# Kernel tuning notes

Measured on AMD Instinct MI355X. Metric: run time of the kernel, lower is better.

Reference implementation:

```python
import jax, jax.numpy as jnp
import numpy as np

B, T, TC = 128, 300, 20          # batch, words per sentence, chars per word
DW, DC = 16, 32                  # word / char embedding dims
UC, UM = 32, 64                  # char-LSTM units, main-LSTM units
POS, PAR = 20, 8                 # extra feature dims
VW, VC = 1834, 132               # vocab sizes
DIN = DW + UC + POS + PAR        # 76, input dim of main BiLSTM


def setup_inputs() -> dict:
    key = jax.random.key(0)
    ks = jax.random.split(key, 16)
    s = 0.05
    f32 = jnp.float32
    return dict(
        word_in=jax.random.randint(ks[0], (B, T), 0, VW, dtype=jnp.int32),
        char_in=jax.random.randint(ks[1], (B, T, TC), 0, VC, dtype=jnp.int32),
        input_pos=jax.random.normal(ks[2], (B, T, POS), f32),
        input_par=jax.random.normal(ks[3], (B, T, PAR), f32),
        emb_wor=jax.random.normal(ks[4], (VW, DW), f32) * s,
        emb_char=jax.random.normal(ks[5], (VC, DC), f32) * s,
        char_Wx=jax.random.normal(ks[6], (DC, 4 * UC), f32) * s,
        char_Wh=jax.random.normal(ks[7], (UC, 4 * UC), f32) * s,
        char_b=jnp.zeros((4 * UC,), f32),
        fwd_Wx=jax.random.normal(ks[8], (DIN, 4 * UM), f32) * s,
        fwd_Wh=jax.random.normal(ks[9], (UM, 4 * UM), f32) * s,
        fwd_b=jnp.zeros((4 * UM,), f32),
        bwd_Wx=jax.random.normal(ks[10], (DIN, 4 * UM), f32) * s,
        bwd_Wh=jax.random.normal(ks[11], (UM, 4 * UM), f32) * s,
        bwd_b=jnp.zeros((4 * UM,), f32),
        dense_W=jax.random.normal(ks[12], (2 * UM, 4), f32) * s,
        dense_b=jnp.zeros((4,), f32),
    )


def _lstm(x, mask, Wx, Wh, b):
    """Masked Keras-style LSTM (gate order i,f,g,o). x:(N,S,D) mask:(N,S) bool.
    Masked steps carry state (Keras mask_zero semantics). Returns (N,S,U)."""
    U = Wh.shape[0]
    xz = jnp.einsum('nsd,df->nsf', x, Wx) + b  # hoist input projection out of scan

    def step(carry, inp):
        h, c = carry
        z_x, m = inp
        z = z_x + h @ Wh
        i, f, g, o = jnp.split(z, 4, axis=-1)
        c_new = jax.nn.sigmoid(f) * c + jax.nn.sigmoid(i) * jnp.tanh(g)
        h_new = jax.nn.sigmoid(o) * jnp.tanh(c_new)
        m = m[:, None]
        h = jnp.where(m, h_new, h)
        c = jnp.where(m, c_new, c)
        return (h, c), h

    N = x.shape[0]
    h0 = jnp.zeros((N, U), x.dtype)
    (_, _), hs = jax.lax.scan(step, (h0, h0),
                              (jnp.swapaxes(xz, 0, 1), jnp.swapaxes(mask, 0, 1)))
    return jnp.swapaxes(hs, 0, 1)


def reference(word_in, char_in, input_pos, input_par,
              emb_wor, emb_char, char_Wx, char_Wh, char_b,
              fwd_Wx, fwd_Wh, fwd_b, bwd_Wx, bwd_Wh, bwd_b,
              dense_W, dense_b):
    # word embeddings: (B,T,DW)
    ew = emb_wor[word_in]
    # char embeddings, TimeDistributed over words: (B*T, TC, DC)
    ec = emb_char[char_in].reshape(B * T, TC, DC)
    cmask = (char_in != 0).reshape(B * T, TC)
    # char LSTM, return_sequences=False -> final (last-valid) state
    ch = _lstm(ec, cmask, char_Wx, char_Wh, char_b)[:, -1, :].reshape(B, T, UC)
    # concat word emb, char encoding, extra features -> (B,T,DIN)
    x = jnp.concatenate([ew, ch, input_pos, input_par], axis=-1)
    wmask = word_in != 0
    hf = _lstm(x, wmask, fwd_Wx, fwd_Wh, fwd_b)
    hb = _lstm(x[:, ::-1], wmask[:, ::-1], bwd_Wx, bwd_Wh, bwd_b)[:, ::-1]
    h = jnp.concatenate([hf, hb], axis=-1)  # (B,T,2*UM)
    return jax.nn.softmax(h @ dense_W + dense_b, axis=-1)  # (B,T,4)
```

## Files before the change

kernel.cpp:

```cpp
#include <hip/hip_runtime.h>
#include <hip/hip_bf16.h>

#define B_ 128
#define T_ 300
#define TC_ 20
#define DW_ 16
#define DC_ 32
#define UC_ 32
#define UM_ 64
#define POS_ 20
#define PAR_ 8
#define VW_ 1834
#define VC_ 132
#define DIN_ 76
#define XS_ 80
#define NROW (B_*T_)

typedef _Float16 half_t;
typedef half_t h2 __attribute__((ext_vector_type(2)));

__device__ __forceinline__ float fast_sig(float x){
  return __builtin_amdgcn_rcpf(1.f + __expf(-x));
}
__device__ __forceinline__ float fast_tanh(float x){
  return __builtin_amdgcn_rcpf(1.f + __expf(-2.f*x))*2.f - 1.f;
}
__device__ __forceinline__ float dot2u(unsigned int a, unsigned int b, float acc){
  union{unsigned int u; h2 h;} x, y; x.u = a; y.u = b;
#if __has_builtin(__builtin_amdgcn_fdot2)
  return __builtin_amdgcn_fdot2(x.h, y.h, acc, false);
#else
  return acc + (float)x.h.x*(float)y.h.x + (float)x.h.y*(float)y.h.y;
#endif
}
__device__ __forceinline__ float us2f(unsigned short s){
  union{unsigned short s; half_t h;} x; x.s = s; return (float)x.h;
}
__device__ __forceinline__ unsigned int packh2(float a, float b){
  union{h2 h; unsigned int u;} cv; cv.h = h2{(half_t)a,(half_t)b}; return cv.u;
}

__global__ void k_prep(const float* __restrict__ emb_char, const float* __restrict__ char_Wx,
                       const float* __restrict__ char_b,  const float* __restrict__ char_Wh,
                       const float* __restrict__ Whf, const float* __restrict__ Whb,
                       const float* __restrict__ Wxf, const float* __restrict__ Wxb,
                       float* __restrict__ xzc, half_t* __restrict__ chT,
                       half_t* __restrict__ whT_h, half_t* __restrict__ wxT_h){
  int id = blockIdx.x*256 + threadIdx.x;
  if (id < 16896){
    int v = id >> 7, j = id & 127;
    float acc = char_b[j];
    #pragma unroll
    for (int k=0;k<DC_;k++) acc += emb_char[v*DC_+k]*char_Wx[k*(4*UC_)+j];
    xzc[id] = acc;
  } else if (id < 20992){
    int t = id - 16896;
    int j = t >> 5, k = t & 31;
    chT[t] = (half_t)char_Wh[k*(4*UC_)+j];
  } else if (id < 53760){
    int t = id - 20992;
    int dirr = t >> 14, j = (t >> 6) & 255, k = t & 63;
    const float* W = dirr ? Whb : Whf;
    whT_h[t] = (half_t)W[k*(4*UM_)+j];
  } else {
    int t = id - 53760;
    int dirr = t / 24576;
    int r = t % 24576;
    int jj = r / 96, k = r % 96;
    const float* W = dirr ? Wxb : Wxf;
    wxT_h[t] = (k < DIN_) ? (half_t)W[k*(4*UM_)+jj] : (half_t)0.f;
  }
}

__global__ __launch_bounds__(512,2) void k_char(const int* __restrict__ char_in,
        const float* __restrict__ xzc, const half_t* __restrict__ chT,
        const int* __restrict__ word_in, const float* __restrict__ emb_wor,
        const float* __restrict__ pos, const float* __restrict__ par,
        float* __restrict__ x){
  __shared__ unsigned int hbuf2[8][16];
  __shared__ float2 zex[8][64];
  __shared__ int sidx[8*TC_];
  const int tid = threadIdx.x;
  const int w8 = tid >> 6;
  const int lane = tid & 63;
  const int u = lane & 31;
  const int half = lane >> 5;
  const int seq = blockIdx.x*8 + w8;

  if (tid < 384){
    int r8 = tid / 48, c48 = tid % 48;
    int row = blockIdx.x*8 + r8;
    int col = (c48 < 16) ? c48 : (c48 + 32);
    float v;
    if (col < DW_)              v = emb_wor[word_in[row]*DW_ + col];
    else if (col < DW_+UC_+POS_) v = pos[row*POS_ + (col-(DW_+UC_))];
    else                         v = par[row*PAR_ + (col-(DW_+UC_+POS_))];
    x[row*XS_ + col] = v;
  }

  if (tid < 8*TC_) sidx[tid] = char_in[blockIdx.x*(8*TC_) + tid];
  if (half==0 && u<16) hbuf2[w8][u] = 0;

  unsigned int wa[16], wb[16];
  {
    const uint4* pa = reinterpret_cast<const uint4*>(chT + (half*64+u)*32);
    const uint4* pb = reinterpret_cast<const uint4*>(chT + (half*64+32+u)*32);
    #pragma unroll
    for (int q=0;q<4;q++){
      uint4 va = pa[q], vb = pb[q];
      wa[q*4+0]=va.x; wa[q*4+1]=va.y; wa[q*4+2]=va.z; wa[q*4+3]=va.w;
      wb[q*4+0]=vb.x; wb[q*4+1]=vb.y; wb[q*4+2]=vb.z; wb[q*4+3]=vb.w;
    }
  }
  __syncthreads();

  float h = 0.f, c = 0.f;
  int idx = sidx[w8*TC_ + 0];
  float za0 = xzc[idx*(4*UC_) + half*64 + u];
  float zb0 = xzc[idx*(4*UC_) + half*64 + 32 + u];

  for (int t=0; t<TC_; t++){
    int idxn = (t+1 < TC_) ? sidx[w8*TC_ + t+1] : 0;
    float zan = xzc[idxn*(4*UC_) + half*64 + u];
    float zbn = xzc[idxn*(4*UC_) + half*64 + 32 + u];

    float za = za0, zb = zb0;
    const uint4* hb = reinterpret_cast<const uint4*>(&hbuf2[w8][0]);
    uint4 q0=hb[0], q1=hb[1], q2=hb[2], q3=hb[3];
    unsigned int hu[16] = {q0.x,q0.y,q0.z,q0.w, q1.x,q1.y,q1.z,q1.w,
                           q2.x,q2.y,q2.z,q2.w, q3.x,q3.y,q3.z,q3.w};
    #pragma unroll
    for (int k=0;k<16;k++){
      za = dot2u(wa[k], hu[k], za);
      zb = dot2u(wb[k], hu[k], zb);
    }
    zex[w8][lane] = make_float2(za, zb);
    if (half == 0){
      float2 p = zex[w8][32+u];
      float zi = za, zf = zb, zg = p.x, zo = p.y;
      float cn = fast_sig(zf)*c + fast_sig(zi)*fast_tanh(zg);
      float hn = fast_sig(zo)*fast_tanh(cn);
      bool m = (idx != 0);
      c = m ? cn : c;
      h = m ? hn : h;
      reinterpret_cast<half_t*>(&hbuf2[w8][0])[u] = (half_t)h;
    }
    idx = idxn; za0 = zan; zb0 = zbn;
  }
  if (half == 0) x[seq*XS_ + DW_ + u] = h;
}

__global__ __launch_bounds__(512,2) void k_xz(const float* __restrict__ x,
      const half_t* __restrict__ wxT_h,
      const float* __restrict__ b_f, const float* __restrict__ b_b,
      half_t* __restrict__ xz){
  __shared__ unsigned int xs[16][40];
  const int j = threadIdx.x;
  const int jj = j & 255;
  const bool bwd = (j >= 256);
  const float bj = bwd ? b_b[jj] : b_f[jj];
  const int u = jj & 63, g = jj >> 6;
  const int ocol = (bwd ? 256 : 0) + u*4 + g;

  unsigned int wq[40];
  {
    const uint4* p = reinterpret_cast<const uint4*>(wxT_h + (size_t)((bwd?256:0)+jj)*96);
    #pragma unroll
    for (int q=0;q<10;q++){
      uint4 v = p[q];
      wq[q*4+0]=v.x; wq[q*4+1]=v.y; wq[q*4+2]=v.z; wq[q*4+3]=v.w;
    }
  }

  const int rowbase = blockIdx.x*16;
  for (int i=j; i<16*40; i+=512){
    int r = i/40, q = i%40;
    unsigned int pk = 0;
    if (q < 38){
      float v0 = x[(size_t)(rowbase+r)*XS_ + 2*q];
      float v1 = x[(size_t)(rowbase+r)*XS_ + 2*q+1];
      pk = packh2(v0, v1);
    }
    xs[r][q] = pk;
  }
  __syncthreads();

  for (int r=0; r<16; r++){
    const uint4* xr = reinterpret_cast<const uint4*>(&xs[r][0]);
    float acc = bj;
    #pragma unroll
    for (int q=0;q<10;q++){
      uint4 v = xr[q];
      acc = dot2u(wq[q*4+0], v.x, acc);
      acc = dot2u(wq[q*4+1], v.y, acc);
      acc = dot2u(wq[q*4+2], v.z, acc);
      acc = dot2u(wq[q*4+3], v.w, acc);
    }
    xz[(size_t)(rowbase+r)*512 + ocol] = (half_t)acc;
  }
}

__global__ __launch_bounds__(64,1) void k_rnn(const half_t* __restrict__ xz,
      const int* __restrict__ word_in, const half_t* __restrict__ whT_h,
      half_t* __restrict__ hcat){
  __shared__ half_t hbuf[64];
  __shared__ int wm[T_];
  const int l = threadIdx.x;
  const int dir = blockIdx.x & 1;
  const int b = blockIdx.x >> 1;

  unsigned int wt[4][32];
  #pragma unroll
  for (int g=0; g<4; g++){
    const uint4* p = reinterpret_cast<const uint4*>(whT_h + ((size_t)dir*256 + g*64 + l)*64);
    #pragma unroll
    for (int q=0;q<8;q++){
      uint4 v = p[q];
      wt[g][q*4+0]=v.x; wt[g][q*4+1]=v.y; wt[g][q*4+2]=v.z; wt[g][q*4+3]=v.w;
    }
  }
  for (int t=l; t<T_; t+=64) wm[t] = word_in[b*T_ + (dir ? (T_-1-t) : t)];
  hbuf[l] = (half_t)0.f;
  __syncthreads();

  float h = 0.f, c_ = 0.f;
  int row0 = b*T_ + (dir ? T_-1 : 0);
  const half_t* xp = xz + (size_t)row0*512 + dir*256 + l*4;
  const ptrdiff_t dstep = dir ? -512 : 512;
  half_t* hout = hcat + (size_t)row0*(2*UM_) + dir*UM_ + l;
  const ptrdiff_t hstep = dir ? -(2*UM_) : (2*UM_);

  ushort4 z0 = *reinterpret_cast<const ushort4*>(xp);
  ushort4 z1 = *reinterpret_cast<const ushort4*>(xp + dstep);
  half_t hh[10];

  for (int outer=0; outer<30; ++outer){
    #pragma unroll
    for (int s=0; s<10; ++s){
      const int t = outer*10 + s;
      ushort4 z2 = {0,0,0,0};
      if (t+2 < T_) z2 = *reinterpret_cast<const ushort4*>(xp + 2*dstep);

      const uint4* hb = reinterpret_cast<const uint4*>(hbuf);
      float ai0=0.f, ai1=0.f, af0=0.f, af1=0.f;
      float ag0=0.f, ag1=0.f, ao0=0.f, ao1=0.f;
      #pragma unroll
      for (int q=0;q<8;q++){
        uint4 hv = hb[q];
        ai0 = dot2u(wt[0][q*4+0], hv.x, ai0); ai1 = dot2u(wt[0][q*4+1], hv.y, ai1);
        ai0 = dot2u(wt[0][q*4+2], hv.z, ai0); ai1 = dot2u(wt[0][q*4+3], hv.w, ai1);
        af0 = dot2u(wt[1][q*4+0], hv.x, af0); af1 = dot2u(wt[1][q*4+1], hv.y, af1);
        af0 = dot2u(wt[1][q*4+2], hv.z, af0); af1 = dot2u(wt[1][q*4+3], hv.w, af1);
        ag0 = dot2u(wt[2][q*4+0], hv.x, ag0); ag1 = dot2u(wt[2][q*4+1], hv.y, ag1);
        ag0 = dot2u(wt[2][q*4+2], hv.z, ag0); ag1 = dot2u(wt[2][q*4+3], hv.w, ag1);
        ao0 = dot2u(wt[3][q*4+0], hv.x, ao0); ao1 = dot2u(wt[3][q*4+1], hv.y, ao1);
        ao0 = dot2u(wt[3][q*4+2], hv.z, ao0); ao1 = dot2u(wt[3][q*4+3], hv.w, ao1);
      }
      float zi = us2f(z0.x) + (ai0+ai1);
      float zf = us2f(z0.y) + (af0+af1);
      float zg = us2f(z0.z) + (ag0+ag1);
      float zo = us2f(z0.w) + (ao0+ao1);

      int mw = wm[t];
      float cn = fast_sig(zf)*c_ + fast_sig(zi)*fast_tanh(zg);
      float hn = fast_sig(zo)*fast_tanh(cn);
      if (mw != 0){ c_ = cn; h = hn; }
      half_t hq = (half_t)h;
      hbuf[l] = hq;
      hh[s] = hq;
      z0 = z1; z1 = z2; xp += dstep;
    }
    #pragma unroll
    for (int s=0; s<10; ++s) hout[(ptrdiff_t)s * hstep] = hh[s];
    hout += (ptrdiff_t)10 * hstep;
  }
}

__global__ void k_dense(const half_t* __restrict__ hcat, const float* __restrict__ W,
                        const float* __restrict__ bias, float* __restrict__ out){
  int r = blockIdx.x*256 + threadIdx.x;
  const uint4* h4 = reinterpret_cast<const uint4*>(hcat + (size_t)r*(2*UM_));
  float a0=bias[0], a1=bias[1], a2=bias[2], a3=bias[3];
  #pragma unroll
  for (int k8=0;k8<16;k8++){
    uint4 v = h4[k8];
    unsigned int uu[4] = {v.x, v.y, v.z, v.w};
    #pragma unroll
    for (int e=0;e<4;e++){
      int k = k8*8 + e*2;
      float hA = us2f((unsigned short)(uu[e] & 0xffffu));
      float hB = us2f((unsigned short)(uu[e] >> 16));
      a0 += hA*W[k*4+0] + hB*W[(k+1)*4+0];
      a1 += hA*W[k*4+1] + hB*W[(k+1)*4+1];
      a2 += hA*W[k*4+2] + hB*W[(k+1)*4+2];
      a3 += hA*W[k*4+3] + hB*W[(k+1)*4+3];
    }
  }
  float mx = fmaxf(fmaxf(a0,a1), fmaxf(a2,a3));
  float e0=__expf(a0-mx), e1=__expf(a1-mx), e2=__expf(a2-mx), e3=__expf(a3-mx);
  float s = __builtin_amdgcn_rcpf(e0+e1+e2+e3);
  out[r*4+0]=e0*s; out[r*4+1]=e1*s; out[r*4+2]=e2*s; out[r*4+3]=e3*s;
}

extern "C" void kernel_launch(void* const* d_in, const int* in_sizes, int n_in,
                              void* d_out, int out_size, void* d_ws, size_t ws_size,
                              hipStream_t stream) {
  const int*   word_in  = (const int*)  d_in[0];
  const int*   char_in  = (const int*)  d_in[1];
  const float* inp_pos  = (const float*)d_in[2];
  const float* inp_par  = (const float*)d_in[3];
  const float* emb_wor  = (const float*)d_in[4];
  const float* emb_char = (const float*)d_in[5];
  const float* char_Wx  = (const float*)d_in[6];
  const float* char_Wh  = (const float*)d_in[7];
  const float* char_b   = (const float*)d_in[8];
  const float* fwd_Wx   = (const float*)d_in[9];
  const float* fwd_Wh   = (const float*)d_in[10];
  const float* fwd_b    = (const float*)d_in[11];
  const float* bwd_Wx   = (const float*)d_in[12];
  const float* bwd_Wh   = (const float*)d_in[13];
  const float* bwd_b    = (const float*)d_in[14];
  const float* dense_W  = (const float*)d_in[15];
  const float* dense_b  = (const float*)d_in[16];
  float* out = (float*)d_out;

  char* base = (char*)d_ws;
  float*  xw    = (float*)base;            base += (size_t)NROW*XS_*4;
  half_t* hcat  = (half_t*)base;           base += (size_t)NROW*128*2;
  float*  xzc   = (float*)base;            base += (size_t)VC_*128*4;
  half_t* chT   = (half_t*)base;           base += 128*32*2;
  half_t* whT_h = (half_t*)base;           base += 2*256*64*2;
  half_t* wxT_h = (half_t*)base;           base += 2*256*96*2;
  half_t* xzw   = (half_t*)base;

  k_prep <<<402, 256, 0, stream>>>(emb_char, char_Wx, char_b, char_Wh,
                                   fwd_Wh, bwd_Wh, fwd_Wx, bwd_Wx,
                                   xzc, chT, whT_h, wxT_h);
  k_char <<<NROW/8, 512, 0, stream>>>(char_in, xzc, chT,
                                      word_in, emb_wor, inp_pos, inp_par, xw);
  k_xz   <<<NROW/16, 512, 0, stream>>>(xw, wxT_h, fwd_b, bwd_b, xzw);
  k_rnn  <<<2*B_, 64, 0, stream>>>(xzw, word_in, whT_h, hcat);
  k_dense<<<NROW/256, 256, 0, stream>>>(hcat, dense_W, dense_b, out);
}
```

Measured before the change: 289.4 us.

## Fuse input projection and recurrence into one kernel with per-chunk flag handoff

Merges the xz projection kernel and the BiLSTM recurrence kernel into a single launch. Producer blocks compute 15-step chunks in an order that matches both directions' consumption, then publish release flags. Consumer chain blocks spin on those flags with acquire loads, so the sequential recurrence can start before all projections finish and the launch gap disappears. The change relies on producer blocks being scheduled before the consumer blocks, which is not guaranteed and could deadlock. Each recurrence block now launches 512 threads but uses only 64 of them.

```diff
diff --git a/kernel.cpp b/kernel.cpp
--- a/kernel.cpp
+++ b/kernel.cpp
@@ -15,6 +15,7 @@
 #define DIN_ 76
 #define XS_ 80
 #define NROW (B_*T_)
+#define NXZB (B_*20)
 
 typedef _Float16 half_t;
 typedef half_t h2 __attribute__((ext_vector_type(2)));
@@ -45,7 +46,8 @@
                        const float* __restrict__ Whf, const float* __restrict__ Whb,
                        const float* __restrict__ Wxf, const float* __restrict__ Wxb,
                        float* __restrict__ xzc, half_t* __restrict__ chT,
-                       half_t* __restrict__ whT_h, half_t* __restrict__ wxT_h){
+                       half_t* __restrict__ whT_h, half_t* __restrict__ wxT_h,
+                       int* __restrict__ flags){
   int id = blockIdx.x*256 + threadIdx.x;
   if (id < 16896){
     int v = id >> 7, j = id & 127;
@@ -62,13 +64,15 @@
     int dirr = t >> 14, j = (t >> 6) & 255, k = t & 63;
     const float* W = dirr ? Whb : Whf;
     whT_h[t] = (half_t)W[k*(4*UM_)+j];
-  } else {
+  } else if (id < 102912){
     int t = id - 53760;
     int dirr = t / 24576;
     int r = t % 24576;
     int jj = r / 96, k = r % 96;
     const float* W = dirr ? Wxb : Wxf;
     wxT_h[t] = (k < DIN_) ? (half_t)W[k*(4*UM_)+jj] : (half_t)0.f;
+  } else if (id < 102912 + NXZB){
+    flags[id - 102912] = 0;
   }
 }
 
@@ -150,64 +154,77 @@
   if (half == 0) x[seq*XS_ + DW_ + u] = h;
 }
 
-__global__ __launch_bounds__(512,2) void k_xz(const float* __restrict__ x,
+__global__ __launch_bounds__(512,2) void k_xzrnn(const float* __restrict__ x,
       const half_t* __restrict__ wxT_h,
       const float* __restrict__ b_f, const float* __restrict__ b_b,
-      half_t* __restrict__ xz){
-  __shared__ unsigned int xs[16][40];
-  const int j = threadIdx.x;
-  const int jj = j & 255;
-  const bool bwd = (j >= 256);
-  const float bj = bwd ? b_b[jj] : b_f[jj];
-  const int u = jj & 63, g = jj >> 6;
-  const int ocol = (bwd ? 256 : 0) + u*4 + g;
-
-  unsigned int wq[40];
-  {
-    const uint4* p = reinterpret_cast<const uint4*>(wxT_h + (size_t)((bwd?256:0)+jj)*96);
-    #pragma unroll
-    for (int q=0;q<10;q++){
-      uint4 v = p[q];
-      wq[q*4+0]=v.x; wq[q*4+1]=v.y; wq[q*4+2]=v.z; wq[q*4+3]=v.w;
-    }
-  }
-
-  const int rowbase = blockIdx.x*16;
-  for (int i=j; i<16*40; i+=512){
-    int r = i/40, q = i%40;
-    unsigned int pk = 0;
-    if (q < 38){
-      float v0 = x[(size_t)(rowbase+r)*XS_ + 2*q];
-      float v1 = x[(size_t)(rowbase+r)*XS_ + 2*q+1];
-      pk = packh2(v0, v1);
-    }
-    xs[r][q] = pk;
-  }
-  __syncthreads();
-
-  for (int r=0; r<16; r++){
-    const uint4* xr = reinterpret_cast<const uint4*>(&xs[r][0]);
-    float acc = bj;
-    #pragma unroll
-    for (int q=0;q<10;q++){
-      uint4 v = xr[q];
-      acc = dot2u(wq[q*4+0], v.x, acc);
-      acc = dot2u(wq[q*4+1], v.y, acc);
-      acc = dot2u(wq[q*4+2], v.z, acc);
-      acc = dot2u(wq[q*4+3], v.w, acc);
-    }
-    xz[(size_t)(rowbase+r)*512 + ocol] = (half_t)acc;
-  }
-}
-
-__global__ __launch_bounds__(64,1) void k_rnn(const half_t* __restrict__ xz,
+      half_t* __restrict__ xz,
       const int* __restrict__ word_in, const half_t* __restrict__ whT_h,
-      half_t* __restrict__ hcat){
+      half_t* __restrict__ hcat, int* __restrict__ flags){
+  const int bid = blockIdx.x;
+  if (bid < NXZB){
+    __shared__ unsigned int xs[15][40];
+    const int oi = bid / B_;
+    const int bi = bid % B_;
+    const int ts = (oi & 1) ? (19 - (oi >> 1)) : (oi >> 1);
+    const int row0 = bi*T_ + ts*15;
+    const int j = threadIdx.x;
+    const int jj = j & 255;
+    const bool bwd = (j >= 256);
+    const float bj = bwd ? b_b[jj] : b_f[jj];
+    const int u = jj & 63, g = jj >> 6;
+    const int ocol = (bwd ? 256 : 0) + u*4 + g;
+
+    unsigned int wq[40];
+    {
+      const uint4* p = reinterpret_cast<const uint4*>(wxT_h + (size_t)((bwd?256:0)+jj)*96);
+      #pragma unroll
+      for (int q=0;q<10;q++){
+        uint4 v = p[q];
+        wq[q*4+0]=v.x; wq[q*4+1]=v.y; wq[q*4+2]=v.z; wq[q*4+3]=v.w;
+      }
+    }
+    for (int i=j; i<15*40; i+=512){
+      int r = i/40, q = i%40;
+      unsigned int pk = 0;
+      if (q < 38){
+        float v0 = x[(size_t)(row0+r)*XS_ + 2*q];
+        float v1 = x[(size_t)(row0+r)*XS_ + 2*q+1];
+        pk = packh2(v0, v1);
+      }
+      xs[r][q] = pk;
+    }
+    __syncthreads();
+
+    #pragma unroll
+    for (int r=0; r<15; r++){
+      const uint4* xr = reinterpret_cast<const uint4*>(&xs[r][0]);
+      float acc = bj;
+      #pragma unroll
+      for (int q=0;q<10;q++){
+        uint4 v = xr[q];
+        acc = dot2u(wq[q*4+0], v.x, acc);
+        acc = dot2u(wq[q*4+1], v.y, acc);
+        acc = dot2u(wq[q*4+2], v.z, acc);
+        acc = dot2u(wq[q*4+3], v.w, acc);
+      }
+      xz[(size_t)(row0+r)*512 + ocol] = (half_t)acc;
+    }
+    __syncthreads();
+    if (j == 0){
+      __threadfence();
+      __hip_atomic_store(&flags[bi*20 + ts], 1, __ATOMIC_RELEASE,
+                         __HIP_MEMORY_SCOPE_AGENT);
+    }
+    return;
+  }
+
+  const int chain = bid - NXZB;
+  if (threadIdx.x >= 64) return;
   __shared__ half_t hbuf[64];
   __shared__ int wm[T_];
   const int l = threadIdx.x;
-  const int dir = blockIdx.x & 1;
-  const int b = blockIdx.x >> 1;
+  const int dir = chain & 1;
+  const int b = chain >> 1;
 
   unsigned int wt[4][32];
   #pragma unroll
@@ -221,7 +238,7 @@
   }
   for (int t=l; t<T_; t+=64) wm[t] = word_in[b*T_ + (dir ? (T_-1-t) : t)];
   hbuf[l] = (half_t)0.f;
-  __syncthreads();
+  __builtin_amdgcn_s_setprio(1);
 
   float h = 0.f, c_ = 0.f;
   int row0 = b*T_ + (dir ? T_-1 : 0);
@@ -230,14 +247,27 @@
   half_t* hout = hcat + (size_t)row0*(2*UM_) + dir*UM_ + l;
   const ptrdiff_t hstep = dir ? -(2*UM_) : (2*UM_);
 
+  {
+    int ts0 = dir ? 19 : 0;
+    const int* fp = flags + b*20 + ts0;
+    while (__hip_atomic_load(fp, __ATOMIC_ACQUIRE, __HIP_MEMORY_SCOPE_AGENT) == 0)
+      __builtin_amdgcn_s_sleep(8);
+  }
   ushort4 z0 = *reinterpret_cast<const ushort4*>(xp);
   ushort4 z1 = *reinterpret_cast<const ushort4*>(xp + dstep);
-  half_t hh[10];
-
-  for (int outer=0; outer<30; ++outer){
-    #pragma unroll
-    for (int s=0; s<10; ++s){
-      const int t = outer*10 + s;
+  half_t hh[15];
+
+  for (int outer=0; outer<20; ++outer){
+    {
+      int on = (outer+1 < 20) ? outer+1 : 19;
+      int tsn = dir ? (19 - on) : on;
+      const int* fp = flags + b*20 + tsn;
+      while (__hip_atomic_load(fp, __ATOMIC_ACQUIRE, __HIP_MEMORY_SCOPE_AGENT) == 0)
+        __builtin_amdgcn_s_sleep(8);
+    }
+    #pragma unroll
+    for (int s=0; s<15; ++s){
+      const int t = outer*15 + s;
       ushort4 z2 = {0,0,0,0};
       if (t+2 < T_) z2 = *reinterpret_cast<const ushort4*>(xp + 2*dstep);
 
@@ -271,8 +301,8 @@
       z0 = z1; z1 = z2; xp += dstep;
     }
     #pragma unroll
-    for (int s=0; s<10; ++s) hout[(ptrdiff_t)s * hstep] = hh[s];
-    hout += (ptrdiff_t)10 * hstep;
+    for (int s=0; s<15; ++s) hout[(ptrdiff_t)s * hstep] = hh[s];
+    hout += (ptrdiff_t)15 * hstep;
   }
 }
 
@@ -331,14 +361,15 @@
   half_t* chT   = (half_t*)base;           base += 128*32*2;
   half_t* whT_h = (half_t*)base;           base += 2*256*64*2;
   half_t* wxT_h = (half_t*)base;           base += 2*256*96*2;
+  int*    flags = (int*)base;              base += NXZB*4;
   half_t* xzw   = (half_t*)base;
 
-  k_prep <<<402, 256, 0, stream>>>(emb_char, char_Wx, char_b, char_Wh,
+  k_prep <<<412, 256, 0, stream>>>(emb_char, char_Wx, char_b, char_Wh,
                                    fwd_Wh, bwd_Wh, fwd_Wx, bwd_Wx,
-                                   xzc, chT, whT_h, wxT_h);
+                                   xzc, chT, whT_h, wxT_h, flags);
   k_char <<<NROW/8, 512, 0, stream>>>(char_in, xzc, chT,
                                       word_in, emb_wor, inp_pos, inp_par, xw);
-  k_xz   <<<NROW/16, 512, 0, stream>>>(xw, wxT_h, fwd_b, bwd_b, xzw);
-  k_rnn  <<<2*B_, 64, 0, stream>>>(xzw, word_in, whT_h, hcat);
+  k_xzrnn<<<NXZB + 2*B_, 512, 0, stream>>>(xw, wxT_h, fwd_b, bwd_b, xzw,
+                                           word_in, whT_h, hcat, flags);
   k_dense<<<NROW/256, 256, 0, stream>>>(hcat, dense_W, dense_b, out);
 }
```

Result: slower. 438.5 us (+51.5%).
